# Performance work log

Measured on AMD Instinct MI355X. Metric: run time of the kernel, lower is better.

The kernel has to match this reference:

```python
import jax, jax.numpy as jnp
import numpy as np

N_NODES = 50000
N_EDGES = 800000
IN_CH = 128
HIDDEN = 32
HEADS = 4
OUT_CH = 128


def _lin_params(key, fan_in, fan_out):
    kw, kb = jax.random.split(key)
    scale = 1.0 / np.sqrt(fan_in)
    W = jax.random.uniform(kw, (fan_in, fan_out), minval=-scale, maxval=scale, dtype=jnp.float32)
    b = jax.random.uniform(kb, (fan_out,), minval=-scale, maxval=scale, dtype=jnp.float32)
    return W, b


def setup_inputs() -> dict:
    key = jax.random.key(0)
    ks = jax.random.split(key, 10)
    x = jax.random.normal(ks[0], (N_NODES, IN_CH), dtype=jnp.float32)
    edge_index = jax.random.randint(ks[1], (2, N_EDGES), 0, N_NODES, dtype=jnp.int64)
    d1 = HIDDEN * HEADS  # 128
    Wq1, bq1 = _lin_params(ks[2], IN_CH, d1)
    Wk1, bk1 = _lin_params(ks[3], IN_CH, d1)
    Wv1, bv1 = _lin_params(ks[4], IN_CH, d1)
    Ws1, bs1 = _lin_params(ks[5], IN_CH, d1)
    Wq2, bq2 = _lin_params(ks[6], d1, OUT_CH)
    Wk2, bk2 = _lin_params(ks[7], d1, OUT_CH)
    Wv2, bv2 = _lin_params(ks[8], d1, OUT_CH)
    Ws2, bs2 = _lin_params(ks[9], d1, OUT_CH)
    return dict(x=x, edge_index=edge_index,
                Wq1=Wq1, bq1=bq1, Wk1=Wk1, bk1=bk1, Wv1=Wv1, bv1=bv1, Ws1=Ws1, bs1=bs1,
                Wq2=Wq2, bq2=bq2, Wk2=Wk2, bk2=bk2, Wv2=Wv2, bv2=bv2, Ws2=Ws2, bs2=bs2)


def transformer_conv(x, src, dst, Wq, bq, Wk, bk, Wv, bv, Ws, bs, heads, n_nodes):
    """PyG TransformerConv (concat=True, beta=False, root_weight=True, dropout=0)."""
    H = heads
    d = Wq.shape[1] // H
    q = (x @ Wq + bq).reshape(n_nodes, H, d)  # [N,H,d]
    k = (x @ Wk + bk).reshape(n_nodes, H, d)
    v = (x @ Wv + bv).reshape(n_nodes, H, d)
    q_e = q[dst]          # [E,H,d] gather by destination (x_i)
    k_e = k[src]          # [E,H,d] gather by source (x_j)
    alpha = jnp.einsum('ehd,ehd->eh', q_e, k_e) / jnp.sqrt(jnp.float32(d))  # [E,H]
    # segment softmax over incoming edges of each destination node
    m = jax.ops.segment_max(alpha, dst, num_segments=n_nodes)  # [N,H]
    m = jnp.where(jnp.isfinite(m), m, 0.0)
    e = jnp.exp(alpha - m[dst])
    denom = jax.ops.segment_sum(e, dst, num_segments=n_nodes)  # [N,H]
    attn = e / (denom[dst] + 1e-16)                            # [E,H]
    msg = v[src] * attn[:, :, None]                            # [E,H,d]
    out = jax.ops.segment_sum(msg, dst, num_segments=n_nodes)  # [N,H,d]
    out = out.reshape(n_nodes, H * d)
    return out + (x @ Ws + bs)  # root/skip connection


def reference(x, edge_index, Wq1, bq1, Wk1, bk1, Wv1, bv1, Ws1, bs1,
              Wq2, bq2, Wk2, bk2, Wv2, bv2, Ws2, bs2):
    src = edge_index[0]
    dst = edge_index[1]
    n = x.shape[0]
    h = transformer_conv(x, src, dst, Wq1, bq1, Wk1, bk1, Wv1, bv1, Ws1, bs1, HEADS, n)
    h = jax.nn.relu(h)
    out = transformer_conv(h, src, dst, Wq2, bq2, Wk2, bk2, Wv2, bv2, Ws2, bs2, 1, n)
    return out
```

## Files before the change

kernel.cpp:

```cpp
#include <hip/hip_runtime.h>

#define N_NODES 50000
#define N_EDGES 800000

typedef __attribute__((ext_vector_type(8))) short bf16x8;
typedef __attribute__((ext_vector_type(4))) float f32x4;

#if __has_builtin(__builtin_amdgcn_fdot2_f32_bf16)
#define HAVE_FDOT2 1
typedef __attribute__((ext_vector_type(2))) __bf16 bf16v2;
#else
#define HAVE_FDOT2 0
#endif

__device__ inline unsigned short f2bf(float f) {
  unsigned int u = __float_as_uint(f);
  unsigned int r = u + 0x7FFFu + ((u >> 16) & 1u);
  return (unsigned short)(r >> 16);
}
__device__ inline float bf_lo(unsigned int u) { return __uint_as_float(u << 16); }
__device__ inline float bf_hi(unsigned int u) { return __uint_as_float(u & 0xffff0000u); }

__global__ void hist_direct(const int* __restrict__ ei, int* __restrict__ cnt) {
  int e = blockIdx.x * 256 + threadIdx.x;
  int hi = ei[2 * e + 1];
  bool is64 = (__ballot(hi == 0) == 0xFFFFFFFFFFFFFFFFull);
  int d = is64 ? ei[2 * (N_EDGES + e)] : ei[N_EDGES + e];
  atomicAdd(&cnt[d], 1);
}

__global__ void scatter_direct(const int* __restrict__ ei, int* __restrict__ cursor,
                               int* __restrict__ ssrc) {
  int e = blockIdx.x * 256 + threadIdx.x;
  int hi = ei[2 * e + 1];
  bool is64 = (__ballot(hi == 0) == 0xFFFFFFFFFFFFFFFFull);
  int s, d;
  if (is64) { s = ei[2 * e]; d = ei[2 * (N_EDGES + e)]; }
  else      { s = ei[e];     d = ei[N_EDGES + e]; }
  int p = atomicAdd(&cursor[d], 1);
  ssrc[p] = s;
}

__device__ inline int block_excl_scan_256(int v, int& total) {
  __shared__ int lds[8];
  int lane = threadIdx.x & 63, wid = threadIdx.x >> 6;
  int orig = v;
#pragma unroll
  for (int off = 1; off < 64; off <<= 1) {
    int t = __shfl_up(v, off);
    if (lane >= off) v += t;
  }
  if (lane == 63) lds[wid] = v;
  __syncthreads();
  if (threadIdx.x == 0) {
    int s = 0;
    for (int w = 0; w < 4; ++w) { int t = lds[w]; lds[w] = s; s += t; }
    lds[4] = s;
  }
  __syncthreads();
  total = lds[4];
  return v + lds[wid] - orig;
}

__global__ __launch_bounds__(256) void scan1(const int* __restrict__ cnt,
                                             int* __restrict__ excl,
                                             int* __restrict__ partials) {
  int i = blockIdx.x * 256 + threadIdx.x;
  int v = (i < N_NODES) ? cnt[i] : 0;
  int total;
  int e = block_excl_scan_256(v, total);
  if (i < N_NODES) excl[i] = e;
  if (threadIdx.x == 0) partials[blockIdx.x] = total;
}

__global__ __launch_bounds__(256) void scan2(int* __restrict__ partials, int nb) {
  int i = threadIdx.x;
  int v = (i < nb) ? partials[i] : 0;
  int total;
  int e = block_excl_scan_256(v, total);
  if (i < nb) partials[i] = e;
}

__global__ __launch_bounds__(256) void scan3(int* __restrict__ row_ptr,
                                             const int* __restrict__ partials,
                                             int* __restrict__ cursor) {
  int i = blockIdx.x * 256 + threadIdx.x;
  if (i < N_NODES) {
    int v = row_ptr[i] + partials[blockIdx.x];
    row_ptr[i] = v;
    cursor[i] = v;
  }
  if (i == 0) row_ptr[N_NODES] = N_EDGES;
}

struct WPack { const float* W[8]; const float* B[8]; };

__global__ void prep_w_both(WPack pk, unsigned short* __restrict__ bt_all,
                            float* __restrict__ bcat_all) {
  int t = blockIdx.x * 256 + threadIdx.x;
  int lay = t >> 16;
  int r = t & 65535;
  int col = r >> 7, kk = r & 127;
  int sel = col >> 7, c = col & 127;
  int idx = lay * 4 + sel;
  const float* W = pk.W[idx];
  bt_all[(size_t)lay * 65536 + col * 128 + kk] = f2bf(W[kk * 128 + c]);
  if (kk == 0) bcat_all[lay * 512 + col] = pk.B[idx][c];
}

template <bool AF32>
__global__ __launch_bounds__(256) void gemm_qkvs(const void* __restrict__ xa,
                                                 const unsigned short* __restrict__ bt,
                                                 const float* __restrict__ bias,
                                                 unsigned short* __restrict__ Oqs,
                                                 unsigned short* __restrict__ Okv) {
  const int wid = threadIdx.x >> 6;
  const int lane = threadIdx.x & 63;
  const int gw = blockIdx.x * 4 + wid;
  const int colGroup = gw & 7;
  const int rowGroup = gw >> 3;
  const int col0 = colGroup * 64;
  const int r = lane & 15;
  const int half = lane >> 4;

  bf16x8 bfrag[4][4];
#pragma unroll
  for (int ct = 0; ct < 4; ++ct) {
    int col = col0 + ct * 16 + r;
    const unsigned short* bp = bt + col * 128 + half * 8;
#pragma unroll
    for (int kc = 0; kc < 4; ++kc)
      bfrag[ct][kc] = *(const bf16x8*)(bp + kc * 32);
  }

#pragma unroll 1
  for (int rt = 0; rt < 5; ++rt) {
    int m0 = (rowGroup * 5 + rt) * 16;
    bf16x8 afrag[4];
    if constexpr (AF32) {
      const float* ap = (const float*)xa + (size_t)(m0 + r) * 128 + half * 8;
#pragma unroll
      for (int kc = 0; kc < 4; ++kc) {
        float4 f0 = *(const float4*)(ap + kc * 32);
        float4 f1 = *(const float4*)(ap + kc * 32 + 4);
        bf16x8 fr;
        fr[0] = (short)f2bf(f0.x); fr[1] = (short)f2bf(f0.y);
        fr[2] = (short)f2bf(f0.z); fr[3] = (short)f2bf(f0.w);
        fr[4] = (short)f2bf(f1.x); fr[5] = (short)f2bf(f1.y);
        fr[6] = (short)f2bf(f1.z); fr[7] = (short)f2bf(f1.w);
        afrag[kc] = fr;
      }
    } else {
      const unsigned short* ap = (const unsigned short*)xa + (size_t)(m0 + r) * 128 + half * 8;
#pragma unroll
      for (int kc = 0; kc < 4; ++kc) afrag[kc] = *(const bf16x8*)(ap + kc * 32);
    }

    f32x4 acc[4] = {{0.f,0.f,0.f,0.f},{0.f,0.f,0.f,0.f},{0.f,0.f,0.f,0.f},{0.f,0.f,0.f,0.f}};
#pragma unroll
    for (int ct = 0; ct < 4; ++ct)
#pragma unroll
      for (int kc = 0; kc < 4; ++kc)
        acc[ct] = __builtin_amdgcn_mfma_f32_16x16x32_bf16(afrag[kc], bfrag[ct][kc], acc[ct], 0, 0, 0);

    int orow = m0 + half * 4;
    if (colGroup < 2) {
#pragma unroll
      for (int ct = 0; ct < 4; ++ct) {
        int col = col0 + ct * 16 + r;
        float bv = bias[col];
#pragma unroll
        for (int j = 0; j < 4; ++j)
          Oqs[(size_t)(orow + j) * 256 + col] = f2bf(acc[ct][j] + bv);
      }
    } else if (colGroup >= 6) {
#pragma unroll
      for (int ct = 0; ct < 4; ++ct) {
        int col = col0 + ct * 16 + r;
        float bv = bias[col];
        int c = col - 384;
#pragma unroll
        for (int j = 0; j < 4; ++j)
          Oqs[(size_t)(orow + j) * 256 + 128 + c] = f2bf(acc[ct][j] + bv);
      }
    } else {
      const int voff  = (colGroup >= 4) ? 2 : 0;
      const int cbase = (colGroup >= 4) ? 256 : 128;
#pragma unroll
      for (int ct = 0; ct < 4; ++ct) {
        int col = col0 + ct * 16 + r;
        float bv = bias[col];
        int c = col - cbase;
        int pos = ((c >> 1) << 2) + voff + (c & 1);
#pragma unroll
        for (int j = 0; j < 4; ++j)
          Okv[(size_t)(orow + j) * 256 + pos] = f2bf(acc[ct][j] + bv);
      }
    }
  }
}

template <int H, bool OUTBF>
__global__ __launch_bounds__(256, 8) void edge_attn(const unsigned short* __restrict__ Oqs,
                                                    const unsigned short* __restrict__ Okv,
                                                    const int* __restrict__ row_ptr,
                                                    const int* __restrict__ ssrc,
                                                    void* __restrict__ outp,
                                                    float scale) {
  int wid = threadIdx.x >> 6, lane = threadIdx.x & 63;
  int n = blockIdx.x * 4 + wid;
  if (n >= N_NODES) return;
  const unsigned int* qsw = (const unsigned int*)Oqs;
  unsigned int qw = qsw[(size_t)n * 128 + lane];
#if HAVE_FDOT2
  const float esc = scale;
  bf16v2 qv = __builtin_bit_cast(bf16v2, qw);
#else
  float qx = bf_lo(qw) * scale, qy = bf_hi(qw) * scale;
#endif
  int start = row_ptr[n], end = row_ptr[n + 1];
  int len = end - start;
  const int* sp = ssrc + start;
  const uint2* kvb = (const uint2*)Okv;
  float acc0 = 0.f, acc1 = 0.f, den = 0.f;

  auto proc = [&](uint2 kv) {
#if HAVE_FDOT2
    float p = __builtin_amdgcn_fdot2_f32_bf16(__builtin_bit_cast(bf16v2, kv.x), qv, 0.f, false);
#else
    float p = qx * bf_lo(kv.x) + qy * bf_hi(kv.x);
#endif
#pragma unroll
    for (int off = 1; off < 64 / H; off <<= 1) p += __shfl_xor(p, off);
#if HAVE_FDOT2
    float e = __expf(p * esc);
#else
    float e = __expf(p);
#endif
    den += e; acc0 += e * bf_lo(kv.y); acc1 += e * bf_hi(kv.y);
  };

  int i = 0;
  if (len >= 8) {
    uint2 a = kvb[(size_t)sp[0] * 64 + lane];
    uint2 b = kvb[(size_t)sp[1] * 64 + lane];
    uint2 c = kvb[(size_t)sp[2] * 64 + lane];
    uint2 d = kvb[(size_t)sp[3] * 64 + lane];
    uint2 e4 = kvb[(size_t)sp[4] * 64 + lane];
    uint2 f = kvb[(size_t)sp[5] * 64 + lane];
    uint2 g = kvb[(size_t)sp[6] * 64 + lane];
    uint2 h = kvb[(size_t)sp[7] * 64 + lane];
    for (i = 8; i + 7 < len; i += 8) {
      uint2 na = kvb[(size_t)sp[i]     * 64 + lane];
      uint2 nb = kvb[(size_t)sp[i + 1] * 64 + lane];
      uint2 nc = kvb[(size_t)sp[i + 2] * 64 + lane];
      uint2 nd = kvb[(size_t)sp[i + 3] * 64 + lane];
      uint2 ne = kvb[(size_t)sp[i + 4] * 64 + lane];
      uint2 nf = kvb[(size_t)sp[i + 5] * 64 + lane];
      uint2 ng = kvb[(size_t)sp[i + 6] * 64 + lane];
      uint2 nh = kvb[(size_t)sp[i + 7] * 64 + lane];
      proc(a); proc(b); proc(c); proc(d); proc(e4); proc(f); proc(g); proc(h);
      a = na; b = nb; c = nc; d = nd; e4 = ne; f = nf; g = ng; h = nh;
    }
    proc(a); proc(b); proc(c); proc(d); proc(e4); proc(f); proc(g); proc(h);
  }
  for (; i < len; ++i) proc(kvb[(size_t)sp[i] * 64 + lane]);

  float inv = 1.0f / (den + 1e-16f);
  unsigned int sw = qsw[(size_t)n * 128 + 64 + lane];
  float r0 = acc0 * inv + bf_lo(sw);
  float r1 = acc1 * inv + bf_hi(sw);
  if (OUTBF) {
    r0 = fmaxf(r0, 0.f); r1 = fmaxf(r1, 0.f);
    unsigned int pk = (unsigned int)f2bf(r0) | ((unsigned int)f2bf(r1) << 16);
    ((unsigned int*)outp)[(size_t)n * 64 + lane] = pk;
  } else {
    ((float2*)outp)[(size_t)n * 64 + lane] = make_float2(r0, r1);
  }
}

extern "C" void kernel_launch(void* const* d_in, const int* in_sizes, int n_in,
                              void* d_out, int out_size, void* d_ws, size_t ws_size,
                              hipStream_t stream) {
  (void)in_sizes; (void)n_in; (void)out_size; (void)ws_size;
  const float* x  = (const float*)d_in[0];
  const int*   ei = (const int*)d_in[1];
  float* out = (float*)d_out;

  char* w = (char*)d_ws;
  size_t off = 0;
  auto alloc = [&](size_t b) { void* p = w + off; off += (b + 255) & ~(size_t)255; return p; };
  int* ssrc   = (int*)alloc((size_t)N_EDGES * 4);
  int* rowp   = (int*)alloc((size_t)(N_NODES + 1) * 4);
  int* cursor = (int*)alloc((size_t)N_NODES * 4);
  int* cnt    = (int*)alloc((size_t)N_NODES * 4);
  int* part   = (int*)alloc(256 * 4);
  unsigned short* xb  = (unsigned short*)alloc((size_t)N_NODES * 128 * 2);
  unsigned short* bt  = (unsigned short*)alloc((size_t)2 * 512 * 128 * 2);
  float* bcat = (float*)alloc(2 * 512 * 4);
  unsigned short* Oqs = (unsigned short*)alloc((size_t)N_NODES * 256 * 2);
  unsigned short* Okv = (unsigned short*)alloc((size_t)N_NODES * 256 * 2);

  WPack pk;
  for (int i = 0; i < 8; ++i) { pk.W[i] = (const float*)d_in[2 + 2 * i]; pk.B[i] = (const float*)d_in[3 + 2 * i]; }

  hipMemsetAsync(cnt, 0, (size_t)N_NODES * 4, stream);
  hist_direct<<<3125, 256, 0, stream>>>(ei, cnt);
  scan1<<<196, 256, 0, stream>>>(cnt, rowp, part);
  scan2<<<1, 256, 0, stream>>>(part, 196);
  scan3<<<196, 256, 0, stream>>>(rowp, part, cursor);
  scatter_direct<<<3125, 256, 0, stream>>>(ei, cursor, ssrc);
  prep_w_both<<<512, 256, 0, stream>>>(pk, bt, bcat);

  gemm_qkvs<true><<<1250, 256, 0, stream>>>(x, bt, bcat, Oqs, Okv);
  edge_attn<4, true><<<12500, 256, 0, stream>>>(Oqs, Okv, rowp, ssrc, xb, 0.17677669529663689f);

  gemm_qkvs<false><<<1250, 256, 0, stream>>>(xb, bt + 65536, bcat + 512, Oqs, Okv);
  edge_attn<1, false><<<12500, 256, 0, stream>>>(Oqs, Okv, rowp, ssrc, out, 0.08838834764831845f);
}
```

Measured before the change: 404.1 us.

## Keep A tile resident per wave and loop over column groups; shrink edge prefetch depth

The QKVS GEMM now assigns each wave one 16-row tile and keeps its A fragments in registers while looping over all eight 64-column groups, reloading B fragments per group instead of keeping B fixed and reloading A for five row tiles. This reads the activation matrix once, which matters most for the fp32 first layer, at the cost of re-reading the small weight matrix from cache eight times per tile. The grid shrinks to 782 blocks and gets a bounds guard. The edge-attention loop's software prefetch depth is also cut from 8 to 4 neighbors, lowering register pressure but exposing more gather latency.

```diff
diff --git a/kernel.cpp b/kernel.cpp
--- a/kernel.cpp
+++ b/kernel.cpp
@@ -2,6 +2,7 @@
 
 #define N_NODES 50000
 #define N_EDGES 800000
+#define N_TILES 3125
 
 typedef __attribute__((ext_vector_type(8))) short bf16x8;
 typedef __attribute__((ext_vector_type(4))) float f32x4;
@@ -116,44 +117,44 @@
                                                  unsigned short* __restrict__ Okv) {
   const int wid = threadIdx.x >> 6;
   const int lane = threadIdx.x & 63;
-  const int gw = blockIdx.x * 4 + wid;
-  const int colGroup = gw & 7;
-  const int rowGroup = gw >> 3;
-  const int col0 = colGroup * 64;
+  const int tile = blockIdx.x * 4 + wid;
+  if (tile >= N_TILES) return;
   const int r = lane & 15;
   const int half = lane >> 4;
-
-  bf16x8 bfrag[4][4];
-#pragma unroll
-  for (int ct = 0; ct < 4; ++ct) {
-    int col = col0 + ct * 16 + r;
-    const unsigned short* bp = bt + col * 128 + half * 8;
-#pragma unroll
-    for (int kc = 0; kc < 4; ++kc)
-      bfrag[ct][kc] = *(const bf16x8*)(bp + kc * 32);
-  }
-
+  const int m0 = tile * 16;
+
+  bf16x8 afrag[4];
+  if constexpr (AF32) {
+    const float* ap = (const float*)xa + (size_t)(m0 + r) * 128 + half * 8;
+#pragma unroll
+    for (int kc = 0; kc < 4; ++kc) {
+      float4 f0 = *(const float4*)(ap + kc * 32);
+      float4 f1 = *(const float4*)(ap + kc * 32 + 4);
+      bf16x8 fr;
+      fr[0] = (short)f2bf(f0.x); fr[1] = (short)f2bf(f0.y);
+      fr[2] = (short)f2bf(f0.z); fr[3] = (short)f2bf(f0.w);
+      fr[4] = (short)f2bf(f1.x); fr[5] = (short)f2bf(f1.y);
+      fr[6] = (short)f2bf(f1.z); fr[7] = (short)f2bf(f1.w);
+      afrag[kc] = fr;
+    }
+  } else {
+    const unsigned short* ap = (const unsigned short*)xa + (size_t)(m0 + r) * 128 + half * 8;
+#pragma unroll
+    for (int kc = 0; kc < 4; ++kc) afrag[kc] = *(const bf16x8*)(ap + kc * 32);
+  }
+
+  const int orow = m0 + half * 4;
 #pragma unroll 1
-  for (int rt = 0; rt < 5; ++rt) {
-    int m0 = (rowGroup * 5 + rt) * 16;
-    bf16x8 afrag[4];
-    if constexpr (AF32) {
-      const float* ap = (const float*)xa + (size_t)(m0 + r) * 128 + half * 8;
-#pragma unroll
-      for (int kc = 0; kc < 4; ++kc) {
-        float4 f0 = *(const float4*)(ap + kc * 32);
-        float4 f1 = *(const float4*)(ap + kc * 32 + 4);
-        bf16x8 fr;
-        fr[0] = (short)f2bf(f0.x); fr[1] = (short)f2bf(f0.y);
-        fr[2] = (short)f2bf(f0.z); fr[3] = (short)f2bf(f0.w);
-        fr[4] = (short)f2bf(f1.x); fr[5] = (short)f2bf(f1.y);
-        fr[6] = (short)f2bf(f1.z); fr[7] = (short)f2bf(f1.w);
-        afrag[kc] = fr;
-      }
-    } else {
-      const unsigned short* ap = (const unsigned short*)xa + (size_t)(m0 + r) * 128 + half * 8;
-#pragma unroll
-      for (int kc = 0; kc < 4; ++kc) afrag[kc] = *(const bf16x8*)(ap + kc * 32);
+  for (int cg = 0; cg < 8; ++cg) {
+    const int col0 = cg * 64;
+    bf16x8 bfrag[4][4];
+#pragma unroll
+    for (int ct = 0; ct < 4; ++ct) {
+      int col = col0 + ct * 16 + r;
+      const unsigned short* bp = bt + col * 128 + half * 8;
+#pragma unroll
+      for (int kc = 0; kc < 4; ++kc)
+        bfrag[ct][kc] = *(const bf16x8*)(bp + kc * 32);
     }
 
     f32x4 acc[4] = {{0.f,0.f,0.f,0.f},{0.f,0.f,0.f,0.f},{0.f,0.f,0.f,0.f},{0.f,0.f,0.f,0.f}};
@@ -163,8 +164,7 @@
       for (int kc = 0; kc < 4; ++kc)
         acc[ct] = __builtin_amdgcn_mfma_f32_16x16x32_bf16(afrag[kc], bfrag[ct][kc], acc[ct], 0, 0, 0);
 
-    int orow = m0 + half * 4;
-    if (colGroup < 2) {
+    if (cg < 2) {
 #pragma unroll
       for (int ct = 0; ct < 4; ++ct) {
         int col = col0 + ct * 16 + r;
@@ -173,7 +173,7 @@
         for (int j = 0; j < 4; ++j)
           Oqs[(size_t)(orow + j) * 256 + col] = f2bf(acc[ct][j] + bv);
       }
-    } else if (colGroup >= 6) {
+    } else if (cg >= 6) {
 #pragma unroll
       for (int ct = 0; ct < 4; ++ct) {
         int col = col0 + ct * 16 + r;
@@ -184,8 +184,8 @@
           Oqs[(size_t)(orow + j) * 256 + 128 + c] = f2bf(acc[ct][j] + bv);
       }
     } else {
-      const int voff  = (colGroup >= 4) ? 2 : 0;
-      const int cbase = (colGroup >= 4) ? 256 : 128;
+      const int voff  = (cg >= 4) ? 2 : 0;
+      const int cbase = (cg >= 4) ? 256 : 128;
 #pragma unroll
       for (int ct = 0; ct < 4; ++ct) {
         int col = col0 + ct * 16 + r;
@@ -241,28 +241,20 @@
   };
 
   int i = 0;
-  if (len >= 8) {
+  if (len >= 4) {
     uint2 a = kvb[(size_t)sp[0] * 64 + lane];
     uint2 b = kvb[(size_t)sp[1] * 64 + lane];
     uint2 c = kvb[(size_t)sp[2] * 64 + lane];
     uint2 d = kvb[(size_t)sp[3] * 64 + lane];
-    uint2 e4 = kvb[(size_t)sp[4] * 64 + lane];
-    uint2 f = kvb[(size_t)sp[5] * 64 + lane];
-    uint2 g = kvb[(size_t)sp[6] * 64 + lane];
-    uint2 h = kvb[(size_t)sp[7] * 64 + lane];
-    for (i = 8; i + 7 < len; i += 8) {
+    for (i = 4; i + 3 < len; i += 4) {
       uint2 na = kvb[(size_t)sp[i]     * 64 + lane];
       uint2 nb = kvb[(size_t)sp[i + 1] * 64 + lane];
       uint2 nc = kvb[(size_t)sp[i + 2] * 64 + lane];
       uint2 nd = kvb[(size_t)sp[i + 3] * 64 + lane];
-      uint2 ne = kvb[(size_t)sp[i + 4] * 64 + lane];
-      uint2 nf = kvb[(size_t)sp[i + 5] * 64 + lane];
-      uint2 ng = kvb[(size_t)sp[i + 6] * 64 + lane];
-      uint2 nh = kvb[(size_t)sp[i + 7] * 64 + lane];
-      proc(a); proc(b); proc(c); proc(d); proc(e4); proc(f); proc(g); proc(h);
-      a = na; b = nb; c = nc; d = nd; e4 = ne; f = nf; g = ng; h = nh;
+      proc(a); proc(b); proc(c); proc(d);
+      a = na; b = nb; c = nc; d = nd;
     }
-    proc(a); proc(b); proc(c); proc(d); proc(e4); proc(f); proc(g); proc(h);
+    proc(a); proc(b); proc(c); proc(d);
   }
   for (; i < len; ++i) proc(kvb[(size_t)sp[i] * 64 + lane]);
 
@@ -312,9 +304,9 @@
   scatter_direct<<<3125, 256, 0, stream>>>(ei, cursor, ssrc);
   prep_w_both<<<512, 256, 0, stream>>>(pk, bt, bcat);
 
-  gemm_qkvs<true><<<1250, 256, 0, stream>>>(x, bt, bcat, Oqs, Okv);
+  gemm_qkvs<true><<<782, 256, 0, stream>>>(x, bt, bcat, Oqs, Okv);
   edge_attn<4, true><<<12500, 256, 0, stream>>>(Oqs, Okv, rowp, ssrc, xb, 0.17677669529663689f);
 
-  gemm_qkvs<false><<<1250, 256, 0, stream>>>(xb, bt + 65536, bcat + 512, Oqs, Okv);
+  gemm_qkvs<false><<<782, 256, 0, stream>>>(xb, bt + 65536, bcat + 512, Oqs, Okv);
   edge_attn<1, false><<<12500, 256, 0, stream>>>(Oqs, Okv, rowp, ssrc, out, 0.08838834764831845f);
 }
```

After: 452.4 us. 11.9% more time.

## Fuse CSR build and weight prep into one cooperative kernel with grid syncs

Applied to the files above, without the earlier changes.

Replaces the memset, histogram, three scan kernels, scatter and weight-prep launches with a single cooperative kernel that separates its phases with grid-wide syncs. This removes several launch gaps between tiny kernels, and the edge-width check is now done once from the first entries rather than by a per-wave ballot. It also halves the software prefetch depth in the edge attention loop from 8 to 4 neighbours, trading memory-level parallelism for fewer registers. Grid syncs and a fixed grid of 1024 blocks may lower throughput in the atomic phases compared with full-size grids.

```diff
diff --git a/kernel.cpp b/kernel.cpp
--- a/kernel.cpp
+++ b/kernel.cpp
@@ -1,7 +1,12 @@
 #include <hip/hip_runtime.h>
+#include <hip/hip_cooperative_groups.h>
+
+namespace cg = cooperative_groups;
 
 #define N_NODES 50000
 #define N_EDGES 800000
+#define COOP_BLOCKS 1024
+#define COOP_NT (COOP_BLOCKS * 256)
 
 typedef __attribute__((ext_vector_type(8))) short bf16x8;
 typedef __attribute__((ext_vector_type(4))) float f32x4;
@@ -21,26 +26,6 @@
 __device__ inline float bf_lo(unsigned int u) { return __uint_as_float(u << 16); }
 __device__ inline float bf_hi(unsigned int u) { return __uint_as_float(u & 0xffff0000u); }
 
-__global__ void hist_direct(const int* __restrict__ ei, int* __restrict__ cnt) {
-  int e = blockIdx.x * 256 + threadIdx.x;
-  int hi = ei[2 * e + 1];
-  bool is64 = (__ballot(hi == 0) == 0xFFFFFFFFFFFFFFFFull);
-  int d = is64 ? ei[2 * (N_EDGES + e)] : ei[N_EDGES + e];
-  atomicAdd(&cnt[d], 1);
-}
-
-__global__ void scatter_direct(const int* __restrict__ ei, int* __restrict__ cursor,
-                               int* __restrict__ ssrc) {
-  int e = blockIdx.x * 256 + threadIdx.x;
-  int hi = ei[2 * e + 1];
-  bool is64 = (__ballot(hi == 0) == 0xFFFFFFFFFFFFFFFFull);
-  int s, d;
-  if (is64) { s = ei[2 * e]; d = ei[2 * (N_EDGES + e)]; }
-  else      { s = ei[e];     d = ei[N_EDGES + e]; }
-  int p = atomicAdd(&cursor[d], 1);
-  ssrc[p] = s;
-}
-
 __device__ inline int block_excl_scan_256(int v, int& total) {
   __shared__ int lds[8];
   int lane = threadIdx.x & 63, wid = threadIdx.x >> 6;
@@ -62,50 +47,78 @@
   return v + lds[wid] - orig;
 }
 
-__global__ __launch_bounds__(256) void scan1(const int* __restrict__ cnt,
-                                             int* __restrict__ excl,
-                                             int* __restrict__ partials) {
-  int i = blockIdx.x * 256 + threadIdx.x;
-  int v = (i < N_NODES) ? cnt[i] : 0;
-  int total;
-  int e = block_excl_scan_256(v, total);
-  if (i < N_NODES) excl[i] = e;
-  if (threadIdx.x == 0) partials[blockIdx.x] = total;
-}
-
-__global__ __launch_bounds__(256) void scan2(int* __restrict__ partials, int nb) {
-  int i = threadIdx.x;
-  int v = (i < nb) ? partials[i] : 0;
-  int total;
-  int e = block_excl_scan_256(v, total);
-  if (i < nb) partials[i] = e;
-}
-
-__global__ __launch_bounds__(256) void scan3(int* __restrict__ row_ptr,
-                                             const int* __restrict__ partials,
-                                             int* __restrict__ cursor) {
-  int i = blockIdx.x * 256 + threadIdx.x;
-  if (i < N_NODES) {
-    int v = row_ptr[i] + partials[blockIdx.x];
-    row_ptr[i] = v;
-    cursor[i] = v;
-  }
-  if (i == 0) row_ptr[N_NODES] = N_EDGES;
-}
-
 struct WPack { const float* W[8]; const float* B[8]; };
 
-__global__ void prep_w_both(WPack pk, unsigned short* __restrict__ bt_all,
-                            float* __restrict__ bcat_all) {
-  int t = blockIdx.x * 256 + threadIdx.x;
-  int lay = t >> 16;
-  int r = t & 65535;
-  int col = r >> 7, kk = r & 127;
-  int sel = col >> 7, c = col & 127;
-  int idx = lay * 4 + sel;
-  const float* W = pk.W[idx];
-  bt_all[(size_t)lay * 65536 + col * 128 + kk] = f2bf(W[kk * 128 + c]);
-  if (kk == 0) bcat_all[lay * 512 + col] = pk.B[idx][c];
+__global__ __launch_bounds__(256) void build_all(const int* __restrict__ ei,
+                                                 int* __restrict__ cnt,
+                                                 int* __restrict__ rowp,
+                                                 int* __restrict__ cursor,
+                                                 int* __restrict__ part,
+                                                 int* __restrict__ ssrc,
+                                                 WPack pk,
+                                                 unsigned short* __restrict__ bt_all,
+                                                 float* __restrict__ bcat_all) {
+  cg::grid_group grid = cg::this_grid();
+  const int tid = blockIdx.x * 256 + threadIdx.x;
+  bool is64 = true;
+#pragma unroll
+  for (int i = 1; i < 16; i += 2) is64 = is64 && (ei[i] == 0);
+
+  for (int i = tid; i < N_NODES; i += COOP_NT) cnt[i] = 0;
+  if (tid < 131072) {
+    int lay = tid >> 16;
+    int r = tid & 65535;
+    int col = r >> 7, kk = r & 127;
+    int sel = col >> 7, c = col & 127;
+    int idx = lay * 4 + sel;
+    bt_all[(size_t)lay * 65536 + col * 128 + kk] = f2bf(pk.W[idx][kk * 128 + c]);
+    if (kk == 0) bcat_all[lay * 512 + col] = pk.B[idx][c];
+  }
+  grid.sync();
+
+  for (int e = tid; e < N_EDGES; e += COOP_NT) {
+    int d = is64 ? ei[2 * (N_EDGES + e)] : ei[N_EDGES + e];
+    atomicAdd(&cnt[d], 1);
+  }
+  grid.sync();
+
+  if (blockIdx.x < 196) {
+    int i = blockIdx.x * 256 + threadIdx.x;
+    int v = (i < N_NODES) ? cnt[i] : 0;
+    int total;
+    int ex = block_excl_scan_256(v, total);
+    if (i < N_NODES) rowp[i] = ex;
+    if (threadIdx.x == 0) part[blockIdx.x] = total;
+  }
+  grid.sync();
+
+  if (blockIdx.x == 0) {
+    int i = threadIdx.x;
+    int v = (i < 196) ? part[i] : 0;
+    int total;
+    int ex = block_excl_scan_256(v, total);
+    if (i < 196) part[i] = ex;
+  }
+  grid.sync();
+
+  if (blockIdx.x < 196) {
+    int i = blockIdx.x * 256 + threadIdx.x;
+    if (i < N_NODES) {
+      int v = rowp[i] + part[blockIdx.x];
+      rowp[i] = v;
+      cursor[i] = v;
+    }
+    if (i == 0) rowp[N_NODES] = N_EDGES;
+  }
+  grid.sync();
+
+  for (int e = tid; e < N_EDGES; e += COOP_NT) {
+    int s, d;
+    if (is64) { s = ei[2 * e]; d = ei[2 * (N_EDGES + e)]; }
+    else      { s = ei[e];     d = ei[N_EDGES + e]; }
+    int p = atomicAdd(&cursor[d], 1);
+    ssrc[p] = s;
+  }
 }
 
 template <bool AF32>
@@ -241,28 +254,20 @@
   };
 
   int i = 0;
-  if (len >= 8) {
+  if (len >= 4) {
     uint2 a = kvb[(size_t)sp[0] * 64 + lane];
     uint2 b = kvb[(size_t)sp[1] * 64 + lane];
     uint2 c = kvb[(size_t)sp[2] * 64 + lane];
     uint2 d = kvb[(size_t)sp[3] * 64 + lane];
-    uint2 e4 = kvb[(size_t)sp[4] * 64 + lane];
-    uint2 f = kvb[(size_t)sp[5] * 64 + lane];
-    uint2 g = kvb[(size_t)sp[6] * 64 + lane];
-    uint2 h = kvb[(size_t)sp[7] * 64 + lane];
-    for (i = 8; i + 7 < len; i += 8) {
+    for (i = 4; i + 3 < len; i += 4) {
       uint2 na = kvb[(size_t)sp[i]     * 64 + lane];
       uint2 nb = kvb[(size_t)sp[i + 1] * 64 + lane];
       uint2 nc = kvb[(size_t)sp[i + 2] * 64 + lane];
       uint2 nd = kvb[(size_t)sp[i + 3] * 64 + lane];
-      uint2 ne = kvb[(size_t)sp[i + 4] * 64 + lane];
-      uint2 nf = kvb[(size_t)sp[i + 5] * 64 + lane];
-      uint2 ng = kvb[(size_t)sp[i + 6] * 64 + lane];
-      uint2 nh = kvb[(size_t)sp[i + 7] * 64 + lane];
-      proc(a); proc(b); proc(c); proc(d); proc(e4); proc(f); proc(g); proc(h);
-      a = na; b = nb; c = nc; d = nd; e4 = ne; f = nf; g = ng; h = nh;
+      proc(a); proc(b); proc(c); proc(d);
+      a = na; b = nb; c = nc; d = nd;
     }
-    proc(a); proc(b); proc(c); proc(d); proc(e4); proc(f); proc(g); proc(h);
+    proc(a); proc(b); proc(c); proc(d);
   }
   for (; i < len; ++i) proc(kvb[(size_t)sp[i] * 64 + lane]);
 
@@ -272,8 +277,8 @@
   float r1 = acc1 * inv + bf_hi(sw);
   if (OUTBF) {
     r0 = fmaxf(r0, 0.f); r1 = fmaxf(r1, 0.f);
-    unsigned int pk = (unsigned int)f2bf(r0) | ((unsigned int)f2bf(r1) << 16);
-    ((unsigned int*)outp)[(size_t)n * 64 + lane] = pk;
+    unsigned int pkv = (unsigned int)f2bf(r0) | ((unsigned int)f2bf(r1) << 16);
+    ((unsigned int*)outp)[(size_t)n * 64 + lane] = pkv;
   } else {
     ((float2*)outp)[(size_t)n * 64 + lane] = make_float2(r0, r1);
   }
@@ -304,13 +309,12 @@
   WPack pk;
   for (int i = 0; i < 8; ++i) { pk.W[i] = (const float*)d_in[2 + 2 * i]; pk.B[i] = (const float*)d_in[3 + 2 * i]; }
 
-  hipMemsetAsync(cnt, 0, (size_t)N_NODES * 4, stream);
-  hist_direct<<<3125, 256, 0, stream>>>(ei, cnt);
-  scan1<<<196, 256, 0, stream>>>(cnt, rowp, part);
-  scan2<<<1, 256, 0, stream>>>(part, 196);
-  scan3<<<196, 256, 0, stream>>>(rowp, part, cursor);
-  scatter_direct<<<3125, 256, 0, stream>>>(ei, cursor, ssrc);
-  prep_w_both<<<512, 256, 0, stream>>>(pk, bt, bcat);
+  {
+    void* args[] = { (void*)&ei, (void*)&cnt, (void*)&rowp, (void*)&cursor,
+                     (void*)&part, (void*)&ssrc, (void*)&pk, (void*)&bt, (void*)&bcat };
+    hipLaunchCooperativeKernel((void*)build_all, dim3(COOP_BLOCKS), dim3(256),
+                               args, 0, stream);
+  }
 
   gemm_qkvs<true><<<1250, 256, 0, stream>>>(x, bt, bcat, Oqs, Okv);
   edge_attn<4, true><<<12500, 256, 0, stream>>>(Oqs, Okv, rowp, ssrc, xb, 0.17677669529663689f);
```

New measurement: 927.9 us. 130% more time.
